# Kernel tuning notes

Measured on AMD Instinct MI355X. Metric: run time of the kernel, lower is better.

Reference implementation:

```python
import jax, jax.numpy as jnp
import numpy as np

PAGE_SIZE = 16
NUM_PAGES = 256
H = 32          # query heads
HKV = 8         # kv heads
D = 128         # head dim
HIDDEN = 4096
SEQ = 2048
ROPE_THETA = 10000.0


def _rope(x, pos):
    # x: [S, h, D], pos: [S]; non-interleaved (rotate-half) RoPE as in
    # flashinfer.rope.apply_rope_pos_ids_inplace / HF Llama.
    half = x.shape[-1] // 2
    inv_freq = 1.0 / (ROPE_THETA ** (jnp.arange(half, dtype=jnp.float32) / half))
    ang = pos.astype(jnp.float32)[:, None] * inv_freq          # [S, half]
    cos = jnp.cos(ang)[:, None, :]
    sin = jnp.sin(ang)[:, None, :]
    x1, x2 = x[..., :half], x[..., half:]
    return jnp.concatenate([x1 * cos - x2 * sin, x2 * cos + x1 * sin], axis=-1).astype(x.dtype)


def setup_inputs() -> dict:
    key = jax.random.key(0)
    ks = jax.random.split(key, 6)
    return {
        "hidden_states": jax.random.normal(ks[0], (1, SEQ, HIDDEN), jnp.float32),
        "position_ids": jnp.arange(SEQ, dtype=jnp.int32),
        "page_indices": jnp.arange(SEQ // PAGE_SIZE, dtype=jnp.int32),  # 128 distinct pages
        "Wq": jax.random.normal(ks[1], (H * D, HIDDEN), jnp.float32) * 0.02,
        "Wk": jax.random.normal(ks[2], (HKV * D, HIDDEN), jnp.float32) * 0.02,
        "Wv": jax.random.normal(ks[3], (HKV * D, HIDDEN), jnp.float32) * 0.02,
        "Wo": jax.random.normal(ks[4], (HIDDEN, H * D), jnp.float32) * 0.02,
        "kv_cache": jnp.zeros((NUM_PAGES, 2, PAGE_SIZE, HKV, D), jnp.float32),
    }


def reference(hidden_states, position_ids, page_indices, Wq, Wk, Wv, Wo, kv_cache):
    S = hidden_states.shape[1]
    x = hidden_states[0]                                  # [S, HIDDEN] (module squeezes batch=1)
    q = (x @ Wq.T).reshape(S, H, D)
    k = (x @ Wk.T).reshape(S, HKV, D)
    v = (x @ Wv.T).reshape(S, HKV, D)
    q = _rope(q, position_ids)
    k = _rope(k, position_ids)

    # Write K/V into the paged cache (page_table.write_block per page)
    n_used = page_indices.shape[0]
    k_pages = k.reshape(n_used, PAGE_SIZE, HKV, D)
    v_pages = v.reshape(n_used, PAGE_SIZE, HKV, D)
    cache = kv_cache.at[page_indices, 0].set(k_pages).at[page_indices, 1].set(v_pages)

    # Gather paged KV back for attention (BatchPrefillWithPagedKVCache)
    kk = cache[page_indices, 0].reshape(-1, HKV, D)[:S]   # [S, HKV, D]
    vv = cache[page_indices, 1].reshape(-1, HKV, D)[:S]

    # GQA: expand kv heads to query heads
    group = H // HKV
    k_rep = jnp.repeat(kk, group, axis=1)                 # [S, H, D]
    v_rep = jnp.repeat(vv, group, axis=1)

    scale = D ** -0.5
    scores = jnp.einsum('qhd,khd->hqk', q * scale, k_rep)  # [H, S, S]
    causal = jnp.arange(S)[:, None] >= jnp.arange(S)[None, :]
    scores = jnp.where(causal[None], scores, jnp.finfo(scores.dtype).min)
    probs = jax.nn.softmax(scores, axis=-1)
    attn = jnp.einsum('hqk,khd->qhd', probs, v_rep)        # [S, H, D]

    out = attn.reshape(S, H * D) @ Wo.T                    # o_proj
    return out[None]                                       # [1, S, HIDDEN]
```

## Files before the change

### kernel.cpp

```cpp
#include <hip/hip_runtime.h>
#include <hip/hip_bf16.h>
#include <math.h>

#define SEQ    2048
#define HIDDEN 4096
#define NH     32
#define NKV    8
#define HD     128
#define QKV_N  6144

typedef __attribute__((ext_vector_type(8))) short bf16x8;
typedef __attribute__((ext_vector_type(4))) float f32x4;
typedef unsigned short u16;
typedef unsigned int u32;

#define VMCNT(n) asm volatile("s_waitcnt vmcnt(" #n ")" ::: "memory")
#define LGKM0 do { asm volatile("s_waitcnt lgkmcnt(0)" ::: "memory"); \
                   __builtin_amdgcn_sched_barrier(0); } while (0)

__device__ inline void gl_lds16(const void* g, void* lds) {
  __builtin_amdgcn_global_load_lds((const __attribute__((address_space(1))) void*)g,
                                   (__attribute__((address_space(3))) void*)lds, 16, 0, 0);
}

__device__ inline void tile_bar() {
  __builtin_amdgcn_sched_barrier(0);
  __builtin_amdgcn_s_barrier();
  __builtin_amdgcn_sched_barrier(0);
}

__device__ inline u16 f2bf(float f) {
  __hip_bfloat16 h = __float2bfloat16(f);
  return *(u16*)&h;
}
__device__ inline float bf2f(u16 u) {
  __hip_bfloat16 h = *(__hip_bfloat16*)&u;
  return __bfloat162float(h);
}

__global__ void cvt_f32_bf16(const float* __restrict__ src, u16* __restrict__ dst, int n8) {
  int i = blockIdx.x * blockDim.x + threadIdx.x;
  if (i >= n8) return;
  const float4* s = (const float4*)src + (size_t)i * 2;
  float4 a = s[0], b = s[1];
  float v[8] = {a.x, a.y, a.z, a.w, b.x, b.y, b.z, b.w};
  union { u16 o[8]; uint4 u; } pk;
#pragma unroll
  for (int j = 0; j < 8; j++) pk.o[j] = f2bf(v[j]);
  *(uint4*)(dst + (size_t)i * 8) = pk.u;
}

template <int OUTF32, int NF>
__global__ __launch_bounds__(512, NF == 2 ? 4 : 2)
void gemm8p(const u16* __restrict__ A, const u16* __restrict__ B,
            void* __restrict__ Cout, int M, int N, int K) {
  constexpr int RING  = (NF == 2) ? 3 : 4;
  constexpr int BROWS = (NF == 2) ? 128 : 256;
  constexpr int A_ELE = 256 * 32;
  constexpr int B_ELE = BROWS * 32;
  __shared__ __align__(16) u16 Ab[RING * A_ELE];
  __shared__ __align__(16) u16 Bb[RING * B_ELE];

  const int tid = threadIdx.x;
  const int w = tid >> 6, lane = tid & 63;
  const int quad = lane >> 4, l16 = lane & 15;
  const int wm = w >> 2, wn = w & 3;
  constexpr int BN = NF * 64;

  const int bid = blockIdx.x;
  const int nbn = N / BN;
  const int npx = nbn >> 3;
  const int n_idx = (bid & 7) * npx + ((bid >> 3) % npx);
  const int m_idx = bid / (8 * npx);
  const int m0 = m_idx * 256, n0 = n_idx * BN;

  const u16* aS = A + (size_t)(m0 + w * 16 + (lane >> 2)) * K + (lane & 3) * 8;
  const u16* bS = B + (size_t)(n0 + w * 16 + (lane >> 2)) * K + (lane & 3) * 8;
  const size_t boff2 = (size_t)((NF == 3 && w >= 4) ? 0 : 128) * K;

  const int NT = K >> 5;

  f32x4 acc[8][NF] = {};

  auto stageA = [&](int t) {
    const int b = t % RING;
    gl_lds16(aS + (size_t)t * 32, &Ab[b * A_ELE + (w * 16) * 32]);
    gl_lds16(aS + (size_t)128 * K + (size_t)t * 32, &Ab[b * A_ELE + (128 + w * 16) * 32]);
  };
  auto stageB = [&](int t) {
    const int b = t % RING;
    gl_lds16(bS + (size_t)t * 32, &Bb[b * B_ELE + (w * 16) * 32]);
    if constexpr (NF == 3)
      gl_lds16(bS + boff2 + (size_t)t * 32, &Bb[b * B_ELE + (128 + w * 16) * 32]);
    if constexpr (NF == 4)
      gl_lds16(bS + (size_t)128 * K + (size_t)t * 32, &Bb[b * B_ELE + (128 + w * 16) * 32]);
  };

  if constexpr (NF == 2) {
    stageA(0); stageB(0); stageA(1); stageB(1);
    VMCNT(3);
  } else {
    stageA(0); stageB(0); stageA(1); stageB(1); stageA(2); stageB(2);
    VMCNT(8);
  }
  tile_bar();

  for (int t = 0; t < NT; ++t) {
    const int b = t % RING;
    const u16* Abt = &Ab[b * A_ELE];
    const u16* Bbt = &Bb[b * B_ELE];

    bf16x8 af0[4], bfv[NF];
#pragma unroll
    for (int f = 0; f < 4; ++f)
      af0[f] = *(const bf16x8*)&Abt[(wm * 128 + f * 16 + l16) * 32 + quad * 8];
#pragma unroll
    for (int n = 0; n < NF; ++n)
      bfv[n] = *(const bf16x8*)&Bbt[(wn * (NF * 16) + n * 16 + l16) * 32 + quad * 8];
    if (t + RING - 1 < NT) stageA(t + RING - 1);
    tile_bar();
    LGKM0;
    __builtin_amdgcn_s_setprio(1);
#pragma unroll
    for (int f = 0; f < 4; ++f)
#pragma unroll
      for (int n = 0; n < NF; ++n)
        acc[f][n] = __builtin_amdgcn_mfma_f32_16x16x32_bf16(af0[f], bfv[n], acc[f][n], 0, 0, 0);
    __builtin_amdgcn_s_setprio(0);
    tile_bar();

    bf16x8 af1[4];
#pragma unroll
    for (int f = 0; f < 4; ++f)
      af1[f] = *(const bf16x8*)&Abt[(wm * 128 + (4 + f) * 16 + l16) * 32 + quad * 8];
    if (t + RING - 1 < NT) stageB(t + RING - 1);
    tile_bar();
    LGKM0;
    __builtin_amdgcn_s_setprio(1);
#pragma unroll
    for (int f = 0; f < 4; ++f)
#pragma unroll
      for (int n = 0; n < NF; ++n)
        acc[4 + f][n] = __builtin_amdgcn_mfma_f32_16x16x32_bf16(af1[f], bfv[n], acc[4 + f][n], 0, 0, 0);
    __builtin_amdgcn_s_setprio(0);

    if (t < NT - 1) {
      if constexpr (NF == 2) {
        if (t + 2 < NT) { VMCNT(3); } else { VMCNT(0); }
      } else {
        if (t + 3 < NT)       { VMCNT(8); }
        else if (t + 3 == NT) { VMCNT(4); }
        else                  { VMCNT(0); }
      }
      tile_bar();
    }
  }

#pragma unroll
  for (int f = 0; f < 8; ++f)
#pragma unroll
    for (int n = 0; n < NF; ++n)
#pragma unroll
      for (int r = 0; r < 4; ++r) {
        int row = m0 + wm * 128 + f * 16 + quad * 4 + r;
        int col = n0 + wn * (NF * 16) + n * 16 + l16;
        float v = acc[f][n][r];
        if (OUTF32) ((float*)Cout)[(size_t)row * N + col] = v;
        else        ((u16*)Cout)[(size_t)row * N + col] = f2bf(v);
      }
}

__global__ void rope_kernel(u16* __restrict__ qkv, const int* __restrict__ pos_ids) {
  int idx = blockIdx.x * blockDim.x + threadIdx.x;
  int d = idx & 63;
  int h = (idx >> 6) % 40;
  int s = idx / (64 * 40);
  if (s >= SEQ) return;
  int off = (h < NH) ? h * HD : HIDDEN + (h - NH) * HD;
  u16* base = qkv + (size_t)s * QKV_N + off;
  float inv_freq = powf(10000.0f, -(float)d * (1.0f / 64.0f));
  float ang = (float)pos_ids[s] * inv_freq;
  float sn, cs;
  sincosf(ang, &sn, &cs);
  float x1 = bf2f(base[d]);
  float x2 = bf2f(base[d + 64]);
  base[d]      = f2bf(x1 * cs - x2 * sn);
  base[d + 64] = f2bf(x2 * cs + x1 * sn);
}

__global__ __launch_bounds__(256) void transpose_v(const u16* __restrict__ qkv,
                                                   u16* __restrict__ vt) {
  __shared__ u16 t[64][72];
  const int s0 = blockIdx.x * 64, c0 = blockIdx.y * 64;
  const int tid = threadIdx.x;
#pragma unroll
  for (int i = 0; i < 2; i++) {
    int r = (tid >> 3) + i * 32;
    int c = (tid & 7) * 8;
    *(uint4*)&t[r][c] = *(const uint4*)&qkv[(size_t)(s0 + r) * QKV_N + 5120 + c0 + c];
  }
  __syncthreads();
#pragma unroll
  for (int i = 0; i < 2; i++) {
    int c = (tid >> 3) + i * 32;
    int s = (tid & 7) * 8;
    union { uint4 u; u16 e[8]; } o;
#pragma unroll
    for (int j = 0; j < 8; j++) o.e[j] = t[s + j][c];
    *(uint4*)&vt[(size_t)(c0 + c) * SEQ + s0 + s] = o.u;
  }
}

__global__ __launch_bounds__(128, 2) void attn_kernel(const u16* __restrict__ qkv,
                                                      const u16* __restrict__ vt,
                                                      u16* __restrict__ attn_out) {
  __shared__ __align__(16) float Ex[32 * 132];
  const int blk = blockIdx.x;
  const int kvh = blk & 7;
  const int hg = (blk >> 3) & 3;
  const int it = 63 - (blk >> 5);
  const int h  = kvh * 4 + hg;
  const int tid = threadIdx.x;
  const int wave = tid >> 6, lane = tid & 63;
  const int quad = lane >> 4, l16 = lane & 15;
  const int q0 = it * 32;

  const float c = 0.08838834764831845f * 1.4426950408889634f;

  bf16x8 qf[2][4];
#pragma unroll
  for (int m = 0; m < 2; m++)
#pragma unroll
    for (int dc = 0; dc < 4; dc++)
      qf[m][dc] = *(const bf16x8*)(qkv + (size_t)(q0 + m * 16 + l16) * QKV_N + h * HD + dc * 32 + quad * 8);

  const u16* kp[4];
#pragma unroll
  for (int st = 0; st < 4; st++)
    kp[st] = qkv + (size_t)(wave * 64 + st * 16 + l16) * QKV_N + HIDDEN + kvh * HD + quad * 8;
  const u16* vp[8];
#pragma unroll
  for (int dt = 0; dt < 8; dt++)
    vp[dt] = vt + (size_t)(kvh * HD + dt * 16 + l16) * SEQ + wave * 64 + quad * 8;

  float lsum[2] = {0.f, 0.f};
  f32x4 o[2][8] = {};

  const int srcA = ((lane >> 4) & 1) * 32 + l16;
  const int srcB = srcA + 16;
  const bool hi = quad >= 2;

  const int n_kt = (q0 + 95) >> 6;

  bf16x8 kbuf[2][4];
#pragma unroll
  for (int dc = 0; dc < 4; dc++) kbuf[0][dc] = *(const bf16x8*)(kp[0] + dc * 32);

  for (int kt = wave; kt < n_kt; kt += 2) {
    const bool last = (kt == n_kt - 1);

    u32 pk[2][4][2];
#pragma unroll
    for (int st = 0; st < 4; st++) {
      const int cb = st & 1;
      const u16* np = (st < 3) ? kp[st + 1] : kp[0] + (size_t)128 * QKV_N;
#pragma unroll
      for (int dc = 0; dc < 4; dc++) kbuf[cb ^ 1][dc] = *(const bf16x8*)(np + dc * 32);
      __builtin_amdgcn_sched_barrier(0);

      f32x4 s[2] = {};
      __builtin_amdgcn_s_setprio(1);
#pragma unroll
      for (int dc = 0; dc < 4; dc++)
#pragma unroll
        for (int m = 0; m < 2; m++)
          s[m] = __builtin_amdgcn_mfma_f32_16x16x32_bf16(kbuf[cb][dc], qf[m][dc], s[m], 0, 0, 0);
      __builtin_amdgcn_s_setprio(0);
#pragma unroll
      for (int m = 0; m < 2; m++) {
        float pr[4];
#pragma unroll
        for (int r = 0; r < 4; r++) {
          float v = fmaf(s[m][r], c, -32.0f);
          if (last) {
            int key = kt * 64 + st * 16 + quad * 4 + r;
            if (key > q0 + m * 16 + l16) v = -1e30f;
          }
          pr[r] = exp2f(v);
          lsum[m] += pr[r];
        }
        pk[m][st][0] = ((u32)f2bf(pr[1]) << 16) | f2bf(pr[0]);
        pk[m][st][1] = ((u32)f2bf(pr[3]) << 16) | f2bf(pr[2]);
      }
    }

    bf16x8 vbuf[8][2];
#pragma unroll
    for (int dt = 0; dt < 4; dt++) {
      vbuf[dt][0] = *(const bf16x8*)(vp[dt]);
      vbuf[dt][1] = *(const bf16x8*)(vp[dt] + 32);
    }
    __builtin_amdgcn_sched_barrier(0);

    bf16x8 pf[2][2];
#pragma unroll
    for (int m = 0; m < 2; m++) {
      if (m == 1) {
#pragma unroll
        for (int dt = 4; dt < 8; dt++) {
          vbuf[dt][0] = *(const bf16x8*)(vp[dt]);
          vbuf[dt][1] = *(const bf16x8*)(vp[dt] + 32);
        }
        __builtin_amdgcn_sched_barrier(0);
      }
#pragma unroll
      for (int kc = 0; kc < 2; kc++) {
        union { u32 w[4]; bf16x8 v; } u;
        u32 a0 = (u32)__shfl((int)pk[m][2 * kc][0],     srcA);
        u32 b0 = (u32)__shfl((int)pk[m][2 * kc + 1][0], srcA);
        u32 a1 = (u32)__shfl((int)pk[m][2 * kc][1],     srcA);
        u32 b1 = (u32)__shfl((int)pk[m][2 * kc + 1][1], srcA);
        u32 a2 = (u32)__shfl((int)pk[m][2 * kc][0],     srcB);
        u32 b2 = (u32)__shfl((int)pk[m][2 * kc + 1][0], srcB);
        u32 a3 = (u32)__shfl((int)pk[m][2 * kc][1],     srcB);
        u32 b3 = (u32)__shfl((int)pk[m][2 * kc + 1][1], srcB);
        u.w[0] = hi ? b0 : a0;
        u.w[1] = hi ? b1 : a1;
        u.w[2] = hi ? b2 : a2;
        u.w[3] = hi ? b3 : a3;
        pf[m][kc] = u.v;
      }
    }

    __builtin_amdgcn_s_setprio(1);
#pragma unroll
    for (int dt = 0; dt < 8; dt++) {
#pragma unroll
      for (int m = 0; m < 2; m++) {
        o[m][dt] = __builtin_amdgcn_mfma_f32_16x16x32_bf16(vbuf[dt][0], pf[m][0], o[m][dt], 0, 0, 0);
        o[m][dt] = __builtin_amdgcn_mfma_f32_16x16x32_bf16(vbuf[dt][1], pf[m][1], o[m][dt], 0, 0, 0);
      }
    }
    __builtin_amdgcn_s_setprio(0);

#pragma unroll
    for (int st = 0; st < 4; st++) kp[st] += (size_t)128 * QKV_N;
#pragma unroll
    for (int dt = 0; dt < 8; dt++) vp[dt] += 128;
  }

#pragma unroll
  for (int m = 0; m < 2; m++) {
    lsum[m] += __shfl_xor(lsum[m], 16);
    lsum[m] += __shfl_xor(lsum[m], 32);
  }

  if (wave == 1) {
#pragma unroll
    for (int m = 0; m < 2; m++) {
#pragma unroll
      for (int dt = 0; dt < 8; dt++)
        *(f32x4*)&Ex[(m * 16 + l16) * 132 + dt * 16 + quad * 4] = o[m][dt];
      if (lane < 16) Ex[(m * 16 + l16) * 132 + 128] = lsum[m];
    }
  }
  __syncthreads();
  if (wave == 0) {
#pragma unroll
    for (int m = 0; m < 2; m++) {
      float lt = lsum[m] + Ex[(m * 16 + l16) * 132 + 128];
      float inv = 1.0f / lt;
      size_t base = (size_t)(q0 + m * 16 + l16) * HIDDEN + h * HD;
#pragma unroll
      for (int dt = 0; dt < 8; dt++) {
        f32x4 p = *(const f32x4*)&Ex[(m * 16 + l16) * 132 + dt * 16 + quad * 4];
        float v0 = (o[m][dt][0] + p[0]) * inv;
        float v1 = (o[m][dt][1] + p[1]) * inv;
        float v2 = (o[m][dt][2] + p[2]) * inv;
        float v3 = (o[m][dt][3] + p[3]) * inv;
        u32 w0 = ((u32)f2bf(v1) << 16) | f2bf(v0);
        u32 w1 = ((u32)f2bf(v3) << 16) | f2bf(v2);
        uint2 wv; wv.x = w0; wv.y = w1;
        *(uint2*)&attn_out[base + dt * 16 + quad * 4] = wv;
      }
    }
  }
}

extern "C" void kernel_launch(void* const* d_in, const int* in_sizes, int n_in,
                              void* d_out, int out_size, void* d_ws, size_t ws_size,
                              hipStream_t stream) {
  const float* x  = (const float*)d_in[0];
  const int* pos  = (const int*)d_in[1];
  const float* Wq = (const float*)d_in[3];
  const float* Wk = (const float*)d_in[4];
  const float* Wv = (const float*)d_in[5];
  const float* Wo = (const float*)d_in[6];
  float* out = (float*)d_out;

  u16* x_bf    = (u16*)d_ws;
  u16* Wqkv_bf = x_bf + (size_t)SEQ * HIDDEN;
  u16* qkv_bf  = Wqkv_bf + (size_t)QKV_N * HIDDEN;
  u16* attn_bf = qkv_bf + (size_t)SEQ * QKV_N;
  u16* Wo_bf   = attn_bf + (size_t)SEQ * HIDDEN;
  u16* vt_bf   = x_bf;

  auto cvt = [&](const float* s, u16* d, size_t n) {
    int n8 = (int)(n / 8);
    cvt_f32_bf16<<<(n8 + 255) / 256, 256, 0, stream>>>(s, d, n8);
  };
  cvt(x,  x_bf,    (size_t)SEQ * HIDDEN);
  cvt(Wq, Wqkv_bf,                         (size_t)4096 * 4096);
  cvt(Wk, Wqkv_bf + (size_t)4096 * 4096,   (size_t)1024 * 4096);
  cvt(Wv, Wqkv_bf + (size_t)5120 * 4096,   (size_t)1024 * 4096);
  cvt(Wo, Wo_bf,   (size_t)4096 * 4096);

  gemm8p<0, 3><<<dim3(256), 512, 0, stream>>>(x_bf, Wqkv_bf, qkv_bf, SEQ, QKV_N, HIDDEN);

  int rope_threads = SEQ * 40 * 64;
  rope_kernel<<<rope_threads / 256, 256, 0, stream>>>(qkv_bf, pos);

  dim3 gt(SEQ / 64, 1024 / 64);
  transpose_v<<<gt, 256, 0, stream>>>(qkv_bf, vt_bf);

  attn_kernel<<<2048, 128, 0, stream>>>(qkv_bf, vt_bf, attn_bf);

  gemm8p<1, 2><<<dim3(256), 512, 0, stream>>>(attn_bf, Wo_bf, out, SEQ, HIDDEN, HIDDEN);
}
```

Measured before the change: 617.9 us.

## Restructure GEMM pipeline to single-barrier stages and reshape o_proj tile to 128x256

The GEMM main loop now issues all A and B global-to-LDS loads for a future stage at once and reads all fragments up front. It uses partial lgkmcnt waits to overlap the second half of the fragment reads with the first MFMA batch, which removes two of the three workgroup barriers per K step. The template gains an MF parameter so the o_proj GEMM uses a 128x256 tile with a 4-deep ring instead of a 256x128 tile with a 3-deep ring. This raises LDS use and lowers the occupancy hint for o_proj to 2, and reading ahead without a barrier depends on the ring depth and vmcnt accounting being correct.

```diff
diff --git a/kernel.cpp b/kernel.cpp
--- a/kernel.cpp
+++ b/kernel.cpp
@@ -15,8 +15,8 @@
 typedef unsigned int u32;
 
 #define VMCNT(n) asm volatile("s_waitcnt vmcnt(" #n ")" ::: "memory")
-#define LGKM0 do { asm volatile("s_waitcnt lgkmcnt(0)" ::: "memory"); \
-                   __builtin_amdgcn_sched_barrier(0); } while (0)
+#define LGKMW(n) do { asm volatile("s_waitcnt lgkmcnt(" #n ")" ::: "memory"); \
+                      __builtin_amdgcn_sched_barrier(0); } while (0)
 
 __device__ inline void gl_lds16(const void* g, void* lds) {
   __builtin_amdgcn_global_load_lds((const __attribute__((address_space(1))) void*)g,
@@ -50,14 +50,16 @@
   *(uint4*)(dst + (size_t)i * 8) = pk.u;
 }
 
-template <int OUTF32, int NF>
-__global__ __launch_bounds__(512, NF == 2 ? 4 : 2)
+template <int OUTF32, int MF, int NF>
+__global__ __launch_bounds__(512, 2)
 void gemm8p(const u16* __restrict__ A, const u16* __restrict__ B,
             void* __restrict__ Cout, int M, int N, int K) {
-  constexpr int RING  = (NF == 2) ? 3 : 4;
-  constexpr int BROWS = (NF == 2) ? 128 : 256;
-  constexpr int A_ELE = 256 * 32;
-  constexpr int B_ELE = BROWS * 32;
+  constexpr int RING   = 4;
+  constexpr int A_ROWS = MF * 32;
+  constexpr int B_LOG  = NF * 64;
+  constexpr int B_ROWS = (NF == 3) ? 256 : B_LOG;
+  constexpr int A_ELE  = A_ROWS * 32;
+  constexpr int B_ELE  = B_ROWS * 32;
   __shared__ __align__(16) u16 Ab[RING * A_ELE];
   __shared__ __align__(16) u16 Bb[RING * B_ELE];
 
@@ -65,44 +67,39 @@
   const int w = tid >> 6, lane = tid & 63;
   const int quad = lane >> 4, l16 = lane & 15;
   const int wm = w >> 2, wn = w & 3;
-  constexpr int BN = NF * 64;
+  constexpr int BN = B_LOG;
 
   const int bid = blockIdx.x;
   const int nbn = N / BN;
   const int npx = nbn >> 3;
   const int n_idx = (bid & 7) * npx + ((bid >> 3) % npx);
   const int m_idx = bid / (8 * npx);
-  const int m0 = m_idx * 256, n0 = n_idx * BN;
+  const int m0 = m_idx * A_ROWS, n0 = n_idx * BN;
 
   const u16* aS = A + (size_t)(m0 + w * 16 + (lane >> 2)) * K + (lane & 3) * 8;
   const u16* bS = B + (size_t)(n0 + w * 16 + (lane >> 2)) * K + (lane & 3) * 8;
   const size_t boff2 = (size_t)((NF == 3 && w >= 4) ? 0 : 128) * K;
 
   const int NT = K >> 5;
-
-  f32x4 acc[8][NF] = {};
-
-  auto stageA = [&](int t) {
+  constexpr int LPT = A_ROWS / 128 + B_ROWS / 128;
+
+  f32x4 acc[MF][NF] = {};
+
+  auto stage = [&](int t) {
     const int b = t % RING;
-    gl_lds16(aS + (size_t)t * 32, &Ab[b * A_ELE + (w * 16) * 32]);
-    gl_lds16(aS + (size_t)128 * K + (size_t)t * 32, &Ab[b * A_ELE + (128 + w * 16) * 32]);
+    const size_t ko = (size_t)t * 32;
+    gl_lds16(aS + ko, &Ab[b * A_ELE + (w * 16) * 32]);
+    if constexpr (A_ROWS == 256)
+      gl_lds16(aS + (size_t)128 * K + ko, &Ab[b * A_ELE + (128 + w * 16) * 32]);
+    gl_lds16(bS + ko, &Bb[b * B_ELE + (w * 16) * 32]);
+    if constexpr (NF == 3)
+      gl_lds16(bS + boff2 + ko, &Bb[b * B_ELE + (128 + w * 16) * 32]);
+    else if constexpr (B_ROWS == 256)
+      gl_lds16(bS + (size_t)128 * K + ko, &Bb[b * B_ELE + (128 + w * 16) * 32]);
   };
-  auto stageB = [&](int t) {
-    const int b = t % RING;
-    gl_lds16(bS + (size_t)t * 32, &Bb[b * B_ELE + (w * 16) * 32]);
-    if constexpr (NF == 3)
-      gl_lds16(bS + boff2 + (size_t)t * 32, &Bb[b * B_ELE + (128 + w * 16) * 32]);
-    if constexpr (NF == 4)
-      gl_lds16(bS + (size_t)128 * K + (size_t)t * 32, &Bb[b * B_ELE + (128 + w * 16) * 32]);
-  };
-
-  if constexpr (NF == 2) {
-    stageA(0); stageB(0); stageA(1); stageB(1);
-    VMCNT(3);
-  } else {
-    stageA(0); stageB(0); stageA(1); stageB(1); stageA(2); stageB(2);
-    VMCNT(8);
-  }
+
+  stage(0); stage(1); stage(2);
+  if constexpr (LPT == 4) { VMCNT(8); } else { VMCNT(6); }
   tile_bar();
 
   for (int t = 0; t < NT; ++t) {
@@ -110,59 +107,58 @@
     const u16* Abt = &Ab[b * A_ELE];
     const u16* Bbt = &Bb[b * B_ELE];
 
-    bf16x8 af0[4], bfv[NF];
-#pragma unroll
-    for (int f = 0; f < 4; ++f)
-      af0[f] = *(const bf16x8*)&Abt[(wm * 128 + f * 16 + l16) * 32 + quad * 8];
+    bf16x8 bfv[NF], af0[MF / 2], af1[MF / 2];
 #pragma unroll
     for (int n = 0; n < NF; ++n)
       bfv[n] = *(const bf16x8*)&Bbt[(wn * (NF * 16) + n * 16 + l16) * 32 + quad * 8];
-    if (t + RING - 1 < NT) stageA(t + RING - 1);
-    tile_bar();
-    LGKM0;
+#pragma unroll
+    for (int f = 0; f < MF / 2; ++f)
+      af0[f] = *(const bf16x8*)&Abt[(wm * (MF * 16) + f * 16 + l16) * 32 + quad * 8];
+#pragma unroll
+    for (int f = 0; f < MF / 2; ++f)
+      af1[f] = *(const bf16x8*)&Abt[(wm * (MF * 16) + (MF / 2 + f) * 16 + l16) * 32 + quad * 8];
+    if (t + 3 < NT) stage(t + 3);
+
+    if constexpr (MF == 8) { LGKMW(4); } else { LGKMW(2); }
     __builtin_amdgcn_s_setprio(1);
 #pragma unroll
-    for (int f = 0; f < 4; ++f)
+    for (int f = 0; f < MF / 2; ++f)
 #pragma unroll
       for (int n = 0; n < NF; ++n)
         acc[f][n] = __builtin_amdgcn_mfma_f32_16x16x32_bf16(af0[f], bfv[n], acc[f][n], 0, 0, 0);
     __builtin_amdgcn_s_setprio(0);
-    tile_bar();
-
-    bf16x8 af1[4];
-#pragma unroll
-    for (int f = 0; f < 4; ++f)
-      af1[f] = *(const bf16x8*)&Abt[(wm * 128 + (4 + f) * 16 + l16) * 32 + quad * 8];
-    if (t + RING - 1 < NT) stageB(t + RING - 1);
-    tile_bar();
-    LGKM0;
+
+    LGKMW(0);
     __builtin_amdgcn_s_setprio(1);
 #pragma unroll
-    for (int f = 0; f < 4; ++f)
+    for (int f = 0; f < MF / 2; ++f)
 #pragma unroll
       for (int n = 0; n < NF; ++n)
-        acc[4 + f][n] = __builtin_amdgcn_mfma_f32_16x16x32_bf16(af1[f], bfv[n], acc[4 + f][n], 0, 0, 0);
+        acc[MF / 2 + f][n] =
+            __builtin_amdgcn_mfma_f32_16x16x32_bf16(af1[f], bfv[n], acc[MF / 2 + f][n], 0, 0, 0);
     __builtin_amdgcn_s_setprio(0);
 
     if (t < NT - 1) {
-      if constexpr (NF == 2) {
-        if (t + 2 < NT) { VMCNT(3); } else { VMCNT(0); }
-      } else {
+      if constexpr (LPT == 4) {
         if (t + 3 < NT)       { VMCNT(8); }
         else if (t + 3 == NT) { VMCNT(4); }
         else                  { VMCNT(0); }
+      } else {
+        if (t + 3 < NT)       { VMCNT(6); }
+        else if (t + 3 == NT) { VMCNT(3); }
+        else                  { VMCNT(0); }
       }
       tile_bar();
     }
   }
 
 #pragma unroll
-  for (int f = 0; f < 8; ++f)
+  for (int f = 0; f < MF; ++f)
 #pragma unroll
     for (int n = 0; n < NF; ++n)
 #pragma unroll
       for (int r = 0; r < 4; ++r) {
-        int row = m0 + wm * 128 + f * 16 + quad * 4 + r;
+        int row = m0 + wm * (MF * 16) + f * 16 + quad * 4 + r;
         int col = n0 + wn * (NF * 16) + n * 16 + l16;
         float v = acc[f][n][r];
         if (OUTF32) ((float*)Cout)[(size_t)row * N + col] = v;
@@ -415,7 +411,7 @@
   cvt(Wv, Wqkv_bf + (size_t)5120 * 4096,   (size_t)1024 * 4096);
   cvt(Wo, Wo_bf,   (size_t)4096 * 4096);
 
-  gemm8p<0, 3><<<dim3(256), 512, 0, stream>>>(x_bf, Wqkv_bf, qkv_bf, SEQ, QKV_N, HIDDEN);
+  gemm8p<0, 8, 3><<<dim3(256), 512, 0, stream>>>(x_bf, Wqkv_bf, qkv_bf, SEQ, QKV_N, HIDDEN);
 
   int rope_threads = SEQ * 40 * 64;
   rope_kernel<<<rope_threads / 256, 256, 0, stream>>>(qkv_bf, pos);
@@ -425,5 +421,5 @@
 
   attn_kernel<<<2048, 128, 0, stream>>>(qkv_bf, vt_bf, attn_bf);
 
-  gemm8p<1, 2><<<dim3(256), 512, 0, stream>>>(attn_bf, Wo_bf, out, SEQ, HIDDEN, HIDDEN);
-}
+  gemm8p<1, 4, 4><<<dim3(256), 512, 0, stream>>>(attn_bf, Wo_bf, out, SEQ, HIDDEN, HIDDEN);
+}
```

New measurement: 579.6 us. 6.2% less time.
